# Kernel tuning notes

Hardware: AMD Instinct MI355X
Metric: run time of the kernel (lower is better)

The kernel has to match this reference:

```python
import jax, jax.numpy as jnp
import numpy as np

ALPHA, BETA, GAMMA = 1.0, 0.5, 0.25
FEATURE_DIM = 4
OHEM_RATIO = 3
K = 8  # fixed number of instance labels (0 = background)
DELTA_V, DELTA_D = 0.5, 1.5
EPS_DICE = 1e-3
EPS_IOU = 1e-6


def setup_inputs() -> dict:
    key = jax.random.key(0)
    k1, k2, k3, k4, k5 = jax.random.split(key, 5)
    B, h, w = 8, 160, 160
    H, W = 4 * h, 4 * w
    maps = jax.random.normal(k1, (B, 2 + FEATURE_DIM, h, w), jnp.float32)
    gt_texts = (jax.random.uniform(k2, (B, H, W)) > 0.5).astype(jnp.float32)
    gt_kernels = (jax.random.uniform(k3, (B, H, W)) > 0.6).astype(jnp.float32)
    training_masks = (jax.random.uniform(k4, (B, H, W)) > 0.05).astype(jnp.float32)
    gt_instance = jax.random.randint(k5, (B, H, W), 0, K).astype(jnp.int32)
    return dict(maps=maps, gt_texts=gt_texts, gt_kernels=gt_kernels,
                gt_instance=gt_instance, training_masks=training_masks)


def _up4(x):
    # F.interpolate(scale_factor=4, mode='nearest')
    return jnp.repeat(jnp.repeat(x, 4, axis=-2), 4, axis=-1)


def _dice(inp, tgt, mask):
    B = inp.shape[0]
    m = mask.reshape(B, -1)
    p = jax.nn.sigmoid(inp).reshape(B, -1) * m
    t = tgt.reshape(B, -1) * m
    a = jnp.sum(p * t, axis=1)
    b = jnp.sum(p * p, axis=1) + EPS_DICE
    c = jnp.sum(t * t, axis=1) + EPS_DICE
    return 1.0 - 2.0 * a / (b + c)  # [B]


def _ohem_single(score, gt, tm):
    pos = gt > 0.5
    pos_num = jnp.sum(pos) - jnp.sum(pos & (tm <= 0.5))
    neg = ~pos
    neg_num = jnp.minimum(pos_num * OHEM_RATIO, jnp.sum(neg))
    neg_scores = jnp.where(neg, score, -jnp.inf).ravel()
    sorted_desc = -jnp.sort(-neg_scores)
    idx = jnp.clip(neg_num - 1, 0, neg_scores.size - 1)
    thr = sorted_desc[idx]
    sel = (((score >= thr) | pos) & (tm > 0.5)).astype(tm.dtype)
    fallback = (pos_num == 0) | (neg_num == 0)
    return jnp.where(fallback, tm, sel)


def _emb_single(emb, instance, kernel, tm):
    # emb: [D,H,W]; EmbLoss v1 (agg/dis/reg), fixed K labels instead of torch.unique
    D = emb.shape[0]
    tm_b = tm > 0.5
    kn_b = kernel > 0.5
    inst = jnp.where(tm_b, instance, 0).ravel()              # instance * training_mask
    inst_k = jnp.where(kn_b & tm_b, instance, 0).ravel()     # instance * kernel
    e = emb.reshape(D, -1)                                   # [D,N]
    labels = jnp.arange(K)
    oh_k = (inst_k[None, :] == labels[:, None]).astype(e.dtype)   # [K,N]
    cnt_k = oh_k.sum(axis=1)                                  # [K]
    emb_mean = jnp.einsum('dn,kn->dk', e, oh_k) / jnp.maximum(cnt_k, 1.0)  # [D,K]
    nz = (labels != 0)
    emb_mean = emb_mean * nz[None, :].astype(e.dtype)          # torch skips lb==0 -> col0 stays 0
    present = cnt_k > 0
    valid = present & nz
    nv = jnp.sum(valid)

    # l_agg: per-pixel distance to own-instance mean
    mean_pix = emb_mean[:, inst]                               # [D,N]
    sqd = jnp.sum((e - mean_pix) ** 2, axis=0)
    dist = jnp.sqrt(jnp.maximum(sqd, 1e-12))
    val = jnp.log(jnp.maximum(dist - DELTA_V, 0.0) ** 2 + 1.0)
    oh_i = (inst[None, :] == labels[:, None]).astype(e.dtype)  # [K,N]
    cnt_i = oh_i.sum(axis=1)
    lagg_per = (oh_i @ val) / jnp.maximum(cnt_i, 1.0)          # [K]
    l_agg = jnp.sum(lagg_per * valid) / jnp.maximum(nv, 1)

    # l_dis: pairwise distances between instance means (off-diag, excl label 0)
    diff = emb_mean[:, :, None] - emb_mean[:, None, :]         # [D,K,K]
    sq = jnp.sum(diff ** 2, axis=0)
    pd = jnp.sqrt(jnp.where(sq > 0, sq, 1.0))                  # safe sqrt; diag masked below
    vdis = jnp.log(jnp.maximum(2.0 * DELTA_D - pd, 0.0) ** 2 + 1.0)
    pmask = (valid[:, None] & valid[None, :] & (~jnp.eye(K, dtype=bool))).astype(e.dtype)
    l_dis = jnp.sum(vdis * pmask) / jnp.maximum(pmask.sum(), 1.0)
    l_dis = jnp.where(nv >= 2, l_dis, 0.0)

    # l_reg over all present labels (col0 is zero -> contributes log(1)=0)
    num_instance = jnp.sum(present)
    l_reg = jnp.sum(jnp.log(jnp.linalg.norm(emb_mean, axis=0) + 1.0) * present) \
            / jnp.maximum(num_instance, 1) * 0.001

    loss = l_agg + l_dis + l_reg
    return jnp.where(nv > 0, loss, 0.0)


def reference(maps, gt_texts, gt_kernels, gt_instance, training_masks):
    p = _up4(maps)                     # [B,6,H,W]
    texts = p[:, 0]
    kernels = p[:, 1]
    embs = p[:, 2:]

    sel = jax.vmap(_ohem_single)(texts, gt_texts, training_masks)
    loss_text = _dice(texts, gt_texts, sel)

    sel_k = (jax.nn.sigmoid(texts) > 0.5).astype(texts.dtype) * training_masks
    loss_kernels = _dice(kernels, gt_kernels, sel_k)

    loss_emb = jax.vmap(_emb_single)(embs, gt_instance, gt_kernels, training_masks)

    loss = ALPHA * loss_text + BETA * loss_kernels + GAMMA * loss_emb  # [B]
    return jnp.mean(loss)  # reduction='mean'
```

## Files before the change

kernel.cpp:

```cpp
#include <hip/hip_runtime.h>
#include <math.h>

#define NB 8
#define CW 160
#define CPB (CW*CW)
#define FW 640
#define PIX (FW*FW)
#define MBLK 25
#define PBLK 400
#define HSUB 8

#define OFF_CNTS     0
#define OFF_CI       (NB*CPB*4)
#define OFF_CKC     (OFF_CI + NB*CPB*8)
#define OFF_PARTM   (OFF_CKC + NB*CPB*8)
#define OFF_PARTV   (OFF_PARTM + NB*MBLK*54*4)
#define OFF_POSNUM  (OFF_PARTV + NB*MBLK*8*4)
#define OFF_HIST0   (OFF_POSNUM + NB*4)
#define OFF_HIST1   (OFF_HIST0 + NB*2048*4)
#define WS_END      (OFF_HIST1 + NB*2048*4)

__device__ __forceinline__ float wredf(float v) {
    #pragma unroll
    for (int o = 32; o; o >>= 1) v += __shfl_xor(v, o, 64);
    return v;
}
__device__ __forceinline__ int wredi(int v) {
    #pragma unroll
    for (int o = 32; o; o >>= 1) v += __shfl_xor(v, o, 64);
    return v;
}
__device__ __forceinline__ unsigned long long wredu64(unsigned long long v) {
    #pragma unroll
    for (int o = 32; o; o >>= 1) v += __shfl_xor(v, o, 64);
    return v;
}
__device__ __forceinline__ unsigned keyxf(float f) {
    unsigned bits = __float_as_uint(f);
    return (bits & 0x80000000u) ? ~bits : (bits | 0x80000000u);
}

__device__ int coscan256(const int* __restrict__ hist, int nbins, int tid, int* s_sum) {
    int chunk = nbins >> 8;
    int base = tid * chunk;
    int s = 0;
    #pragma unroll 8
    for (int i = 0; i < chunk; i++) s += hist[base + i];
    s_sum[tid] = s;
    __syncthreads();
    #pragma unroll
    for (int off = 1; off < 256; off <<= 1) {
        int add = (tid >= off) ? s_sum[tid - off] : 0;
        __syncthreads();
        s_sum[tid] += add;
        __syncthreads();
    }
    return s_sum[255];
}
__device__ void cofind256(const int* __restrict__ hist, int nbins, int tid,
                          const int* s_sum, int j, int* s_out) {
    int chunk = nbins >> 8;
    if (tid == 0) { s_out[0] = 0; s_out[1] = 0; }
    __syncthreads();
    int incl = s_sum[tid];
    int excl = (tid > 0) ? s_sum[tid - 1] : 0;
    if (j >= excl && j < incl) {
        int base = tid * chunk, cum = excl;
        for (int i = 0; i < chunk; i++) {
            int c = hist[base + i];
            if (j < cum + c) { s_out[0] = base + i; s_out[1] = j - cum; break; }
            cum += c;
        }
    }
    __syncthreads();
}
__device__ __forceinline__ int ohem_j(int pn, int N) {
    long long nn = min(3LL * (long long)pn, (long long)N);
    int j = (int)((long long)N - nn);
    if (j < 0) j = 0;
    if (j >= N) j = (N > 0) ? N - 1 : 0;
    return j;
}

__global__ __launch_bounds__(256) void k_pass1(const float* __restrict__ gt_texts,
                                               const float* __restrict__ gt_kernels,
                                               const int*   __restrict__ gt_instance,
                                               const float* __restrict__ tm,
                                               unsigned* __restrict__ cnts,
                                               unsigned long long* __restrict__ ciA,
                                               unsigned long long* __restrict__ ckA,
                                               int* __restrict__ posNum,
                                               int* __restrict__ hist0,
                                               int* __restrict__ hist1) {
    int tid = threadIdx.x;
    if (blockIdx.x < 64) {
        int zi = blockIdx.x * 256 + tid;
        hist0[zi] = 0;
        hist1[zi] = 0;
        if (zi < NB) posNum[zi] = 0;
    }
    int b = blockIdx.x / PBLK;
    int blk = blockIdx.x - b * PBLK;
    int r = tid >> 6;
    int c = tid & 63;
    int cp = blk * 64 + c;
    int cy = cp / CW, cx = cp - cy * CW;
    size_t fbase = (size_t)b * PIX + (size_t)(cy * 4 + r) * FW + cx * 4;

    float4 g  = *reinterpret_cast<const float4*>(gt_texts   + fbase);
    float4 gk = *reinterpret_cast<const float4*>(gt_kernels + fbase);
    float4 m  = *reinterpret_cast<const float4*>(tm         + fbase);
    int4  idv = *reinterpret_cast<const int4*>(gt_instance + fbase);

    int neg = 0, c_tmb = 0, c_gt = 0, c_kb = 0;
    unsigned long long ci = 0, ck = 0;
    auto px = [&](float gg, float gkk, float mm, int id) {
        bool tmb = mm > 0.5f;
        bool gt  = gg > 0.5f;
        bool gkb = gkk > 0.5f;
        neg += !gt;
        c_tmb += tmb;
        c_gt += (gt && tmb);
        bool kb = tmb && gkb;
        c_kb += kb;
        ci += 1ull << ((tmb ? id : 0) * 8);
        ck += 1ull << ((kb ? id : 0) * 8);
    };
    px(g.x, gk.x, m.x, idv.x);
    px(g.y, gk.y, m.y, idv.y);
    px(g.z, gk.z, m.z, idv.z);
    px(g.w, gk.w, m.w, idv.w);

    __shared__ unsigned long long s_ci[256];
    __shared__ unsigned long long s_ck[256];
    __shared__ unsigned s_cnt[256];
    s_ci[tid] = ci;
    s_ck[tid] = ck;
    s_cnt[tid] = (unsigned)c_tmb | ((unsigned)c_gt << 8) | ((unsigned)c_kb << 16) | ((unsigned)neg << 24);
    __syncthreads();
    if (tid < 64) {
        unsigned cs = s_cnt[tid] + s_cnt[tid + 64] + s_cnt[tid + 128] + s_cnt[tid + 192];
        unsigned long long cis = s_ci[tid] + s_ci[tid + 64] + s_ci[tid + 128] + s_ci[tid + 192];
        unsigned long long cks = s_ck[tid] + s_ck[tid + 64] + s_ck[tid + 128] + s_ck[tid + 192];
        int gidx = b * CPB + blk * 64 + tid;
        cnts[gidx] = cs;
        ciA[gidx] = cis;
        ckA[gidx] = cks;
    }
}

__global__ __launch_bounds__(256) void k_hist0(const float* __restrict__ maps,
                                               const unsigned* __restrict__ cnts,
                                               int* __restrict__ posNum,
                                               int* __restrict__ hist0) {
    int b = blockIdx.x >> 3, hb = blockIdx.x & 7, tid = threadIdx.x;
    const float* tex = maps + (size_t)b * 6 * CPB;
    const unsigned* cn = cnts + b * CPB;
    __shared__ int h[2048];
    for (int i = tid; i < 2048; i += 256) h[i] = 0;
    __syncthreads();
    int posSum = 0;
    #pragma unroll
    for (int it = 0; it < 4; it++) {
        int q = it * 256 + tid;
        if (q < 800) {
            int i0 = hb * 3200 + q * 4;
            float4 t4 = *reinterpret_cast<const float4*>(tex + i0);
            uint4  c4 = *reinterpret_cast<const uint4*>(cn + i0);
            float tv[4] = {t4.x, t4.y, t4.z, t4.w};
            unsigned cv[4] = {c4.x, c4.y, c4.z, c4.w};
            #pragma unroll
            for (int j = 0; j < 4; j++) {
                posSum += (int)((cv[j] >> 8) & 255);
                int w = (int)(cv[j] >> 24);
                if (w) atomicAdd(&h[keyxf(tv[j]) >> 21], w);
            }
        }
    }
    posSum = wredi(posSum);
    if ((tid & 63) == 0 && posSum) atomicAdd(&posNum[b], posSum);
    __syncthreads();
    for (int i = tid; i < 2048; i += 256) {
        int v = h[i];
        if (v) atomicAdd(&hist0[b * 2048 + i], v);
    }
}

__global__ __launch_bounds__(256) void k_hist1(const float* __restrict__ maps,
                                               const unsigned* __restrict__ cnts,
                                               const int* __restrict__ posNum,
                                               const int* __restrict__ hist0,
                                               int* __restrict__ hist1) {
    int b = blockIdx.x >> 3, hb = blockIdx.x & 7, tid = threadIdx.x;
    __shared__ int s_sum[256], s_out[2];
    const int* h0 = hist0 + b * 2048;
    int N = coscan256(h0, 2048, tid, s_sum);
    int j0 = ohem_j(posNum[b], N);
    cofind256(h0, 2048, tid, s_sum, j0, s_out);
    int d0 = s_out[0];
    __shared__ int h[2048];
    for (int i = tid; i < 2048; i += 256) h[i] = 0;
    __syncthreads();
    const float* tex = maps + (size_t)b * 6 * CPB;
    const unsigned* cn = cnts + b * CPB;
    #pragma unroll
    for (int it = 0; it < 4; it++) {
        int q = it * 256 + tid;
        if (q < 800) {
            int i0 = hb * 3200 + q * 4;
            float4 t4 = *reinterpret_cast<const float4*>(tex + i0);
            uint4  c4 = *reinterpret_cast<const uint4*>(cn + i0);
            float tv[4] = {t4.x, t4.y, t4.z, t4.w};
            unsigned cv[4] = {c4.x, c4.y, c4.z, c4.w};
            #pragma unroll
            for (int j = 0; j < 4; j++) {
                int w = (int)(cv[j] >> 24);
                if (!w) continue;
                unsigned key = keyxf(tv[j]);
                if ((int)(key >> 21) == d0) atomicAdd(&h[(key >> 10) & 0x7FF], w);
            }
        }
    }
    __syncthreads();
    for (int i = tid; i < 2048; i += 256) {
        int v = h[i];
        if (v) atomicAdd(&hist1[b * 2048 + i], v);
    }
}

__global__ __launch_bounds__(256) void k_main_c(const float* __restrict__ maps,
                                                const unsigned* __restrict__ cnts,
                                                const unsigned long long* __restrict__ ciA,
                                                const unsigned long long* __restrict__ ckA,
                                                const int* __restrict__ posNum,
                                                const int* __restrict__ hist0,
                                                const int* __restrict__ hist1,
                                                float* __restrict__ partM) {
    int b = blockIdx.x / MBLK;
    int blk = blockIdx.x - b * MBLK;
    int tid = threadIdx.x;
    int p0 = (blk * 256 + tid) * 4;
    const float* mb = maps + (size_t)b * 6 * CPB;

    float txa[4], kna[4], e0a[4], e1a[4], e2a[4], e3a[4];
    *reinterpret_cast<float4*>(txa) = *reinterpret_cast<const float4*>(mb + p0);
    *reinterpret_cast<float4*>(kna) = *reinterpret_cast<const float4*>(mb + CPB + p0);
    *reinterpret_cast<float4*>(e0a) = *reinterpret_cast<const float4*>(mb + 2 * CPB + p0);
    *reinterpret_cast<float4*>(e1a) = *reinterpret_cast<const float4*>(mb + 3 * CPB + p0);
    *reinterpret_cast<float4*>(e2a) = *reinterpret_cast<const float4*>(mb + 4 * CPB + p0);
    *reinterpret_cast<float4*>(e3a) = *reinterpret_cast<const float4*>(mb + 5 * CPB + p0);
    unsigned ca[4];
    *reinterpret_cast<uint4*>(ca) = *reinterpret_cast<const uint4*>(cnts + b * CPB + p0);
    unsigned long long cia[4], cka[4];
    *reinterpret_cast<ulonglong2*>(cia)     = *reinterpret_cast<const ulonglong2*>(ciA + b * CPB + p0);
    *reinterpret_cast<ulonglong2*>(cia + 2) = *reinterpret_cast<const ulonglong2*>(ciA + b * CPB + p0 + 2);
    *reinterpret_cast<ulonglong2*>(cka)     = *reinterpret_cast<const ulonglong2*>(ckA + b * CPB + p0);
    *reinterpret_cast<ulonglong2*>(cka + 2) = *reinterpret_cast<const ulonglong2*>(ckA + b * CPB + p0 + 2);

    __shared__ int s_sum[256], s_out[2];
    const int* h0 = hist0 + b * 2048;
    const int* h1 = hist1 + b * 2048;
    int N = coscan256(h0, 2048, tid, s_sum);
    int pn = posNum[b];
    long long nn = min(3LL * (long long)pn, (long long)N);
    int fb = (pn == 0 || nn == 0) ? 1 : 0;
    int j0 = ohem_j(pn, N);
    cofind256(h0, 2048, tid, s_sum, j0, s_out);
    int d0 = s_out[0], j1 = s_out[1];
    coscan256(h1, 2048, tid, s_sum);
    cofind256(h1, 2048, tid, s_sum, j1, s_out);
    int d1 = s_out[0];
    unsigned key = ((unsigned)d0 << 21) | ((unsigned)d1 << 10);
    unsigned tb = (key & 0x80000000u) ? (key & 0x7FFFFFFFu) : ~key;
    float thr = __uint_as_float(tb);

    float at = 0.f, bt = 0.f, ct = 0.f, ak = 0.f, bk = 0.f, ckd = 0.f;
    unsigned long long ciS = 0, ckS = 0;
    float se[4][8];
    #pragma unroll
    for (int d = 0; d < 4; d++)
        #pragma unroll
        for (int k = 0; k < 8; k++) se[d][k] = 0.f;

    #pragma unroll
    for (int j = 0; j < 4; j++) {
        float tx = txa[j], kn = kna[j];
        unsigned c = ca[j];
        float c_tmb = (float)(c & 255);
        float c_gt  = (float)((c >> 8) & 255);
        float c_kb  = (float)((c >> 16) & 255);
        float sig_t = 1.f / (1.f + expf(-tx));
        float sig_k = 1.f / (1.f + expf(-kn));
        bool sge = (tx >= thr);
        bool skp = (tx > 0.0f);
        float n_sel = fb ? c_tmb : (sge ? c_tmb : c_gt);
        float n_selk = skp ? c_tmb : 0.f;
        float n_selk_g = skp ? c_kb : 0.f;
        at += sig_t * c_gt;
        bt += sig_t * sig_t * n_sel;
        ct += c_gt;
        ak += sig_k * n_selk_g;
        bk += sig_k * sig_k * n_selk;
        ckd += n_selk_g;
        ciS += cia[j];
        unsigned long long ck = cka[j];
        ckS += ck;
        #pragma unroll
        for (int k = 1; k < 8; k++) {
            float fc = (float)((ck >> (8 * k)) & 255);
            se[0][k] += e0a[j] * fc;
            se[1][k] += e1a[j] * fc;
            se[2][k] += e2a[j] * fc;
            se[3][k] += e3a[j] * fc;
        }
    }

    at = wredf(at); bt = wredf(bt); ct = wredf(ct);
    ak = wredf(ak); bk = wredf(bk); ckd = wredf(ckd);
    const unsigned long long M = 0x00FF00FF00FF00FFull;
    unsigned long long ci0 = wredu64(ciS & M);
    unsigned long long ci1 = wredu64((ciS >> 8) & M);
    unsigned long long ck0 = wredu64(ckS & M);
    unsigned long long ck1 = wredu64((ckS >> 8) & M);
    #pragma unroll
    for (int d = 0; d < 4; d++)
        #pragma unroll
        for (int k = 1; k < 8; k++) se[d][k] = wredf(se[d][k]);

    __shared__ float sh[4][54];
    int w = tid >> 6;
    if ((tid & 63) == 0) {
        sh[w][0] = at; sh[w][1] = bt; sh[w][2] = ct;
        sh[w][3] = ak; sh[w][4] = bk; sh[w][5] = ckd;
        #pragma unroll
        for (int q = 0; q < 4; q++) {
            sh[w][6 + 2 * q]      = (float)((ck0 >> (16 * q)) & 0xFFFF);
            sh[w][6 + 2 * q + 1]  = (float)((ck1 >> (16 * q)) & 0xFFFF);
            sh[w][14 + 2 * q]     = (float)((ci0 >> (16 * q)) & 0xFFFF);
            sh[w][14 + 2 * q + 1] = (float)((ci1 >> (16 * q)) & 0xFFFF);
        }
        #pragma unroll
        for (int d = 0; d < 4; d++) {
            sh[w][22 + d * 8] = 0.f;
            #pragma unroll
            for (int k = 1; k < 8; k++) sh[w][22 + d * 8 + k] = se[d][k];
        }
    }
    __syncthreads();
    if (tid < 54)
        partM[(size_t)(b * MBLK + blk) * 54 + tid] =
            sh[0][tid] + sh[1][tid] + sh[2][tid] + sh[3][tid];
}

__global__ __launch_bounds__(256) void k_val_c(const float* __restrict__ maps,
                                               const unsigned long long* __restrict__ ciA,
                                               const float* __restrict__ partM,
                                               float* __restrict__ partV) {
    int b = blockIdx.x / MBLK;
    int blk = blockIdx.x - b * MBLK;
    int tid = threadIdx.x;
    int p0 = (blk * 256 + tid) * 4;
    const float* mb = maps + (size_t)b * 6 * CPB;

    float e0a[4], e1a[4], e2a[4], e3a[4];
    *reinterpret_cast<float4*>(e0a) = *reinterpret_cast<const float4*>(mb + 2 * CPB + p0);
    *reinterpret_cast<float4*>(e1a) = *reinterpret_cast<const float4*>(mb + 3 * CPB + p0);
    *reinterpret_cast<float4*>(e2a) = *reinterpret_cast<const float4*>(mb + 4 * CPB + p0);
    *reinterpret_cast<float4*>(e3a) = *reinterpret_cast<const float4*>(mb + 5 * CPB + p0);
    unsigned long long cia[4];
    *reinterpret_cast<ulonglong2*>(cia)     = *reinterpret_cast<const ulonglong2*>(ciA + b * CPB + p0);
    *reinterpret_cast<ulonglong2*>(cia + 2) = *reinterpret_cast<const ulonglong2*>(ciA + b * CPB + p0 + 2);

    __shared__ float A54[54];
    __shared__ float shm[32];
    __shared__ float shv[8];
    if (tid < 54) {
        float s = 0.f;
        #pragma unroll 5
        for (int j = 0; j < MBLK; j++) s += partM[(size_t)(b * MBLK + j) * 54 + tid];
        A54[tid] = s;
    }
    __syncthreads();
    if (tid < 32) {
        int k = tid & 7;
        shm[tid] = (k == 0) ? 0.f : A54[22 + tid] / fmaxf(A54[6 + k], 1.f);
    }
    if (tid < 8) shv[tid] = (tid != 0 && A54[6 + tid] > 0.f) ? 1.f : 0.f;
    __syncthreads();

    float sv[8];
    #pragma unroll
    for (int k = 0; k < 8; k++) sv[k] = 0.f;
    #pragma unroll
    for (int j = 0; j < 4; j++) {
        unsigned long long ci = cia[j];
        #pragma unroll
        for (int k = 1; k < 8; k++) {
            int c = (int)((ci >> (8 * k)) & 255);
            if (c && shv[k] > 0.5f) {
                float d0 = e0a[j] - shm[k], d1 = e1a[j] - shm[8 + k];
                float d2 = e2a[j] - shm[16 + k], d3 = e3a[j] - shm[24 + k];
                float sq = d0 * d0 + d1 * d1 + d2 * d2 + d3 * d3;
                float dist = sqrtf(fmaxf(sq, 1e-12f));
                float t = fmaxf(dist - 0.5f, 0.f);
                sv[k] += logf(t * t + 1.f) * (float)c;
            }
        }
    }
    #pragma unroll
    for (int k = 1; k < 8; k++) sv[k] = wredf(sv[k]);
    __shared__ float shp[4][8];
    int w = tid >> 6;
    if ((tid & 63) == 0) {
        shp[w][0] = 0.f;
        #pragma unroll
        for (int k = 1; k < 8; k++) shp[w][k] = sv[k];
    }
    __syncthreads();
    if (tid < 8)
        partV[(size_t)(b * MBLK + blk) * 8 + tid] =
            shp[0][tid] + shp[1][tid] + shp[2][tid] + shp[3][tid];
}

__global__ __launch_bounds__(64) void k_final(const float* __restrict__ partM,
                                              const float* __restrict__ partV,
                                              float* __restrict__ out) {
    int tid = threadIdx.x;
    __shared__ float AM[NB][54];
    __shared__ float SV[NB][8];
    __shared__ float tot[NB];
    for (int i = tid; i < NB * 54; i += 64) {
        int b = i / 54, c = i - b * 54;
        float s = 0.f;
        for (int j = 0; j < MBLK; j++) s += partM[(size_t)(b * MBLK + j) * 54 + c];
        AM[b][c] = s;
    }
    {
        int b = tid >> 3, k = tid & 7;
        float s = 0.f;
        for (int j = 0; j < MBLK; j++) s += partV[(size_t)(b * MBLK + j) * 8 + k];
        SV[b][k] = s;
    }
    __syncthreads();
    if (tid < NB) {
        int b = tid;
        const float* A = AM[b];
        float ltext = 1.f - 2.f * A[0] / (A[1] + A[2] + 0.002f);
        float lkern = 1.f - 2.f * A[3] / (A[4] + A[5] + 0.002f);
        float m[4][8];
        float valid[8];
        int nv = 0, ninst = 0;
        #pragma unroll
        for (int k = 0; k < 8; k++) {
            float c = A[6 + k];
            float inv = 1.f / fmaxf(c, 1.f);
            #pragma unroll
            for (int d = 0; d < 4; d++) m[d][k] = (k == 0) ? 0.f : A[22 + d * 8 + k] * inv;
            int pres = (c > 0.f);
            ninst += pres;
            int v = pres && (k != 0);
            nv += v;
            valid[k] = (float)v;
        }
        float s = 0.f;
        for (int i = 1; i < 8; i++) {
            if (valid[i] < 0.5f) continue;
            for (int j = 1; j < 8; j++) {
                if (j == i || valid[j] < 0.5f) continue;
                float sq = 0.f;
                #pragma unroll
                for (int d = 0; d < 4; d++) { float df = m[d][i] - m[d][j]; sq += df * df; }
                float pd = sqrtf(sq > 0.f ? sq : 1.f);
                float t = fmaxf(3.f - pd, 0.f);
                s += logf(t * t + 1.f);
            }
        }
        float pairs = (float)(nv * nv - nv);
        float l_dis = (nv >= 2) ? s / fmaxf(pairs, 1.f) : 0.f;
        float s2 = 0.f;
        for (int k = 0; k < 8; k++) {
            if (A[6 + k] > 0.f) {
                float n2 = 0.f;
                #pragma unroll
                for (int d = 0; d < 4; d++) n2 += m[d][k] * m[d][k];
                s2 += logf(sqrtf(n2) + 1.f);
            }
        }
        float l_reg = s2 / fmaxf((float)ninst, 1.f) * 0.001f;
        float lagg = 0.f;
        #pragma unroll
        for (int k = 0; k < 8; k++)
            lagg += valid[k] * (SV[b][k] / fmaxf(A[14 + k], 1.f));
        lagg /= fmaxf((float)nv, 1.f);
        float le = (nv > 0) ? (lagg + l_dis + l_reg) : 0.f;
        tot[b] = ltext + 0.5f * lkern + 0.25f * le;
    }
    __syncthreads();
    if (tid == 0) {
        float t = 0.f;
        for (int b = 0; b < NB; b++) t += tot[b];
        out[0] = t / (float)NB;
    }
}

extern "C" void kernel_launch(void* const* d_in, const int* in_sizes, int n_in,
                              void* d_out, int out_size, void* d_ws, size_t ws_size,
                              hipStream_t stream) {
    const float* maps        = (const float*)d_in[0];
    const float* gt_texts    = (const float*)d_in[1];
    const float* gt_kernels  = (const float*)d_in[2];
    const int*   gt_instance = (const int*)d_in[3];
    const float* tm          = (const float*)d_in[4];
    char* ws = (char*)d_ws;
    unsigned* cnts  = (unsigned*)(ws + OFF_CNTS);
    unsigned long long* ciA = (unsigned long long*)(ws + OFF_CI);
    unsigned long long* ckA = (unsigned long long*)(ws + OFF_CKC);
    float* partM    = (float*)(ws + OFF_PARTM);
    float* partV    = (float*)(ws + OFF_PARTV);
    int*   posNum   = (int*)(ws + OFF_POSNUM);
    int*   hist0    = (int*)(ws + OFF_HIST0);
    int*   hist1    = (int*)(ws + OFF_HIST1);

    k_pass1<<<NB * PBLK, 256, 0, stream>>>(gt_texts, gt_kernels, gt_instance, tm,
                                           cnts, ciA, ckA, posNum, hist0, hist1);
    k_hist0<<<NB * HSUB, 256, 0, stream>>>(maps, cnts, posNum, hist0);
    k_hist1<<<NB * HSUB, 256, 0, stream>>>(maps, cnts, posNum, hist0, hist1);
    k_main_c<<<NB * MBLK, 256, 0, stream>>>(maps, cnts, ciA, ckA, posNum, hist0, hist1, partM);
    k_val_c<<<NB * MBLK, 256, 0, stream>>>(maps, ciA, partM, partV);
    k_final<<<1, 64, 0, stream>>>(partM, partV, (float*)d_out);
}
```

Baseline: 138.5 us.

## Fuse all loss stages into one cooperative persistent kernel with grid syncs

Replaces the six-kernel pipeline with a single cooperative kernel of 512 persistent blocks that loops over the work of each former kernel, separated by grid-wide syncs. The aim is to remove launch gaps and per-kernel tail effects between the small histogram, main and final stages. The first OHEM histogram search is now done once per batch and stored as threshold metadata, so the main stage no longer rescans the first-level histogram. Risks: grid.sync cost, fewer blocks for the bandwidth-heavy first pass, and the old multi-kernel path kept as a fallback if the cooperative launch fails.

```diff
diff --git a/kernel.cpp b/kernel.cpp
--- a/kernel.cpp
+++ b/kernel.cpp
@@ -1,5 +1,8 @@
 #include <hip/hip_runtime.h>
+#include <hip/hip_cooperative_groups.h>
 #include <math.h>
+
+namespace cg = cooperative_groups;
 
 #define NB 8
 #define CW 160
@@ -9,6 +12,7 @@
 #define MBLK 25
 #define PBLK 400
 #define HSUB 8
+#define GRID 512
 
 #define OFF_CNTS     0
 #define OFF_CI       (NB*CPB*4)
@@ -18,7 +22,8 @@
 #define OFF_POSNUM  (OFF_PARTV + NB*MBLK*8*4)
 #define OFF_HIST0   (OFF_POSNUM + NB*4)
 #define OFF_HIST1   (OFF_HIST0 + NB*2048*4)
-#define WS_END      (OFF_HIST1 + NB*2048*4)
+#define OFF_META    (OFF_HIST1 + NB*2048*4)
+#define WS_END      (OFF_META + NB*16)
 
 __device__ __forceinline__ float wredf(float v) {
     #pragma unroll
@@ -80,6 +85,427 @@
     if (j < 0) j = 0;
     if (j >= N) j = (N > 0) ? N - 1 : 0;
     return j;
+}
+
+__global__ __launch_bounds__(256, 2) void k_fused(const float* __restrict__ gt_texts,
+                                                  const float* __restrict__ gt_kernels,
+                                                  const int*   __restrict__ gt_instance,
+                                                  const float* __restrict__ tm,
+                                                  const float* __restrict__ maps,
+                                                  unsigned* __restrict__ cnts,
+                                                  unsigned long long* __restrict__ ciA,
+                                                  unsigned long long* __restrict__ ckA,
+                                                  int* __restrict__ posNum,
+                                                  int* __restrict__ hist0,
+                                                  int* __restrict__ hist1,
+                                                  int* __restrict__ thrMeta,
+                                                  float* __restrict__ partM,
+                                                  float* __restrict__ partV,
+                                                  float* __restrict__ out) {
+    cg::grid_group grid = cg::this_grid();
+    const int tid = threadIdx.x;
+    const int nbk = gridDim.x;
+
+    __shared__ int h[2048];
+    __shared__ int s_sum[256];
+    __shared__ int s_out[2];
+    __shared__ unsigned long long s_ci[256];
+    __shared__ unsigned long long s_ck[256];
+    __shared__ unsigned s_cnt[256];
+
+    for (int i = blockIdx.x * 256 + tid; i < NB * 2048; i += nbk * 256) {
+        hist0[i] = 0;
+        hist1[i] = 0;
+    }
+    if (blockIdx.x == 0 && tid < NB) posNum[tid] = 0;
+
+    for (int u = blockIdx.x; u < NB * PBLK; u += nbk) {
+        int b = u / PBLK;
+        int blk = u - b * PBLK;
+        int r = tid >> 6;
+        int c = tid & 63;
+        int cp = blk * 64 + c;
+        int cy = cp / CW, cx = cp - cy * CW;
+        size_t fbase = (size_t)b * PIX + (size_t)(cy * 4 + r) * FW + cx * 4;
+
+        float4 g  = *reinterpret_cast<const float4*>(gt_texts   + fbase);
+        float4 gk = *reinterpret_cast<const float4*>(gt_kernels + fbase);
+        float4 m  = *reinterpret_cast<const float4*>(tm         + fbase);
+        int4  idv = *reinterpret_cast<const int4*>(gt_instance + fbase);
+
+        int neg = 0, c_tmb = 0, c_gt = 0, c_kb = 0;
+        unsigned long long ci = 0, ck = 0;
+        auto px = [&](float gg, float gkk, float mm, int id) {
+            bool tmb = mm > 0.5f;
+            bool gt  = gg > 0.5f;
+            bool gkb = gkk > 0.5f;
+            neg += !gt;
+            c_tmb += tmb;
+            c_gt += (gt && tmb);
+            bool kb = tmb && gkb;
+            c_kb += kb;
+            ci += 1ull << ((tmb ? id : 0) * 8);
+            ck += 1ull << ((kb ? id : 0) * 8);
+        };
+        px(g.x, gk.x, m.x, idv.x);
+        px(g.y, gk.y, m.y, idv.y);
+        px(g.z, gk.z, m.z, idv.z);
+        px(g.w, gk.w, m.w, idv.w);
+
+        s_ci[tid] = ci;
+        s_ck[tid] = ck;
+        s_cnt[tid] = (unsigned)c_tmb | ((unsigned)c_gt << 8) | ((unsigned)c_kb << 16) | ((unsigned)neg << 24);
+        __syncthreads();
+        if (tid < 64) {
+            unsigned cs = s_cnt[tid] + s_cnt[tid + 64] + s_cnt[tid + 128] + s_cnt[tid + 192];
+            unsigned long long cis = s_ci[tid] + s_ci[tid + 64] + s_ci[tid + 128] + s_ci[tid + 192];
+            unsigned long long cks = s_ck[tid] + s_ck[tid + 64] + s_ck[tid + 128] + s_ck[tid + 192];
+            int gidx = b * CPB + blk * 64 + tid;
+            cnts[gidx] = cs;
+            ciA[gidx] = cis;
+            ckA[gidx] = cks;
+        }
+        __syncthreads();
+    }
+    grid.sync();
+
+    for (int u = blockIdx.x; u < NB * HSUB; u += nbk) {
+        int b = u >> 3, hb = u & 7;
+        const float* tex = maps + (size_t)b * 6 * CPB;
+        const unsigned* cn = cnts + b * CPB;
+        for (int i = tid; i < 2048; i += 256) h[i] = 0;
+        __syncthreads();
+        int posSum = 0;
+        #pragma unroll
+        for (int it = 0; it < 4; it++) {
+            int q = it * 256 + tid;
+            if (q < 800) {
+                int i0 = hb * 3200 + q * 4;
+                float4 t4 = *reinterpret_cast<const float4*>(tex + i0);
+                uint4  c4 = *reinterpret_cast<const uint4*>(cn + i0);
+                float tv[4] = {t4.x, t4.y, t4.z, t4.w};
+                unsigned cv[4] = {c4.x, c4.y, c4.z, c4.w};
+                #pragma unroll
+                for (int j = 0; j < 4; j++) {
+                    posSum += (int)((cv[j] >> 8) & 255);
+                    int w = (int)(cv[j] >> 24);
+                    if (w) atomicAdd(&h[keyxf(tv[j]) >> 21], w);
+                }
+            }
+        }
+        posSum = wredi(posSum);
+        if ((tid & 63) == 0 && posSum) atomicAdd(&posNum[b], posSum);
+        __syncthreads();
+        for (int i = tid; i < 2048; i += 256) {
+            int v = h[i];
+            if (v) atomicAdd(&hist0[b * 2048 + i], v);
+        }
+        __syncthreads();
+    }
+    grid.sync();
+
+    for (int u = blockIdx.x; u < NB * HSUB; u += nbk) {
+        int b = u >> 3, hb = u & 7;
+        const int* h0 = hist0 + b * 2048;
+        int N = coscan256(h0, 2048, tid, s_sum);
+        int pn = posNum[b];
+        long long nn = min(3LL * (long long)pn, (long long)N);
+        int fb = (pn == 0 || nn == 0) ? 1 : 0;
+        int j0 = ohem_j(pn, N);
+        cofind256(h0, 2048, tid, s_sum, j0, s_out);
+        int d0 = s_out[0], j1 = s_out[1];
+        if (hb == 0 && tid == 0) {
+            thrMeta[b * 4]     = d0;
+            thrMeta[b * 4 + 1] = j1;
+            thrMeta[b * 4 + 2] = fb;
+        }
+        for (int i = tid; i < 2048; i += 256) h[i] = 0;
+        __syncthreads();
+        const float* tex = maps + (size_t)b * 6 * CPB;
+        const unsigned* cn = cnts + b * CPB;
+        #pragma unroll
+        for (int it = 0; it < 4; it++) {
+            int q = it * 256 + tid;
+            if (q < 800) {
+                int i0 = hb * 3200 + q * 4;
+                float4 t4 = *reinterpret_cast<const float4*>(tex + i0);
+                uint4  c4 = *reinterpret_cast<const uint4*>(cn + i0);
+                float tv[4] = {t4.x, t4.y, t4.z, t4.w};
+                unsigned cv[4] = {c4.x, c4.y, c4.z, c4.w};
+                #pragma unroll
+                for (int j = 0; j < 4; j++) {
+                    int w = (int)(cv[j] >> 24);
+                    if (!w) continue;
+                    unsigned key = keyxf(tv[j]);
+                    if ((int)(key >> 21) == d0) atomicAdd(&h[(key >> 10) & 0x7FF], w);
+                }
+            }
+        }
+        __syncthreads();
+        for (int i = tid; i < 2048; i += 256) {
+            int v = h[i];
+            if (v) atomicAdd(&hist1[b * 2048 + i], v);
+        }
+        __syncthreads();
+    }
+    grid.sync();
+
+    for (int u = blockIdx.x; u < NB * MBLK; u += nbk) {
+        int b = u / MBLK;
+        int blk = u - b * MBLK;
+        int p0 = (blk * 256 + tid) * 4;
+        const float* mb = maps + (size_t)b * 6 * CPB;
+
+        float txa[4], kna[4], e0a[4], e1a[4], e2a[4], e3a[4];
+        *reinterpret_cast<float4*>(txa) = *reinterpret_cast<const float4*>(mb + p0);
+        *reinterpret_cast<float4*>(kna) = *reinterpret_cast<const float4*>(mb + CPB + p0);
+        *reinterpret_cast<float4*>(e0a) = *reinterpret_cast<const float4*>(mb + 2 * CPB + p0);
+        *reinterpret_cast<float4*>(e1a) = *reinterpret_cast<const float4*>(mb + 3 * CPB + p0);
+        *reinterpret_cast<float4*>(e2a) = *reinterpret_cast<const float4*>(mb + 4 * CPB + p0);
+        *reinterpret_cast<float4*>(e3a) = *reinterpret_cast<const float4*>(mb + 5 * CPB + p0);
+        unsigned ca[4];
+        *reinterpret_cast<uint4*>(ca) = *reinterpret_cast<const uint4*>(cnts + b * CPB + p0);
+        unsigned long long cia[4], cka[4];
+        *reinterpret_cast<ulonglong2*>(cia)     = *reinterpret_cast<const ulonglong2*>(ciA + b * CPB + p0);
+        *reinterpret_cast<ulonglong2*>(cia + 2) = *reinterpret_cast<const ulonglong2*>(ciA + b * CPB + p0 + 2);
+        *reinterpret_cast<ulonglong2*>(cka)     = *reinterpret_cast<const ulonglong2*>(ckA + b * CPB + p0);
+        *reinterpret_cast<ulonglong2*>(cka + 2) = *reinterpret_cast<const ulonglong2*>(ckA + b * CPB + p0 + 2);
+
+        int d0 = thrMeta[b * 4], j1 = thrMeta[b * 4 + 1], fb = thrMeta[b * 4 + 2];
+        const int* h1 = hist1 + b * 2048;
+        coscan256(h1, 2048, tid, s_sum);
+        cofind256(h1, 2048, tid, s_sum, j1, s_out);
+        int d1 = s_out[0];
+        unsigned key = ((unsigned)d0 << 21) | ((unsigned)d1 << 10);
+        unsigned tb = (key & 0x80000000u) ? (key & 0x7FFFFFFFu) : ~key;
+        float thr = __uint_as_float(tb);
+
+        float at = 0.f, bt = 0.f, ct = 0.f, ak = 0.f, bk = 0.f, ckd = 0.f;
+        unsigned long long ciS = 0, ckS = 0;
+        float se[4][8];
+        #pragma unroll
+        for (int d = 0; d < 4; d++)
+            #pragma unroll
+            for (int k = 0; k < 8; k++) se[d][k] = 0.f;
+
+        #pragma unroll
+        for (int j = 0; j < 4; j++) {
+            float tx = txa[j], kn = kna[j];
+            unsigned c = ca[j];
+            float c_tmb = (float)(c & 255);
+            float c_gt  = (float)((c >> 8) & 255);
+            float c_kb  = (float)((c >> 16) & 255);
+            float sig_t = 1.f / (1.f + expf(-tx));
+            float sig_k = 1.f / (1.f + expf(-kn));
+            bool sge = (tx >= thr);
+            bool skp = (tx > 0.0f);
+            float n_sel = fb ? c_tmb : (sge ? c_tmb : c_gt);
+            float n_selk = skp ? c_tmb : 0.f;
+            float n_selk_g = skp ? c_kb : 0.f;
+            at += sig_t * c_gt;
+            bt += sig_t * sig_t * n_sel;
+            ct += c_gt;
+            ak += sig_k * n_selk_g;
+            bk += sig_k * sig_k * n_selk;
+            ckd += n_selk_g;
+            ciS += cia[j];
+            unsigned long long ck = cka[j];
+            ckS += ck;
+            #pragma unroll
+            for (int k = 1; k < 8; k++) {
+                float fc = (float)((ck >> (8 * k)) & 255);
+                se[0][k] += e0a[j] * fc;
+                se[1][k] += e1a[j] * fc;
+                se[2][k] += e2a[j] * fc;
+                se[3][k] += e3a[j] * fc;
+            }
+        }
+
+        at = wredf(at); bt = wredf(bt); ct = wredf(ct);
+        ak = wredf(ak); bk = wredf(bk); ckd = wredf(ckd);
+        const unsigned long long M = 0x00FF00FF00FF00FFull;
+        unsigned long long ci0 = wredu64(ciS & M);
+        unsigned long long ci1 = wredu64((ciS >> 8) & M);
+        unsigned long long ck0 = wredu64(ckS & M);
+        unsigned long long ck1 = wredu64((ckS >> 8) & M);
+        #pragma unroll
+        for (int d = 0; d < 4; d++)
+            #pragma unroll
+            for (int k = 1; k < 8; k++) se[d][k] = wredf(se[d][k]);
+
+        float* shf = (float*)h;
+        int w = tid >> 6;
+        if ((tid & 63) == 0) {
+            float* sw = shf + w * 54;
+            sw[0] = at; sw[1] = bt; sw[2] = ct;
+            sw[3] = ak; sw[4] = bk; sw[5] = ckd;
+            #pragma unroll
+            for (int q = 0; q < 4; q++) {
+                sw[6 + 2 * q]      = (float)((ck0 >> (16 * q)) & 0xFFFF);
+                sw[6 + 2 * q + 1]  = (float)((ck1 >> (16 * q)) & 0xFFFF);
+                sw[14 + 2 * q]     = (float)((ci0 >> (16 * q)) & 0xFFFF);
+                sw[14 + 2 * q + 1] = (float)((ci1 >> (16 * q)) & 0xFFFF);
+            }
+            #pragma unroll
+            for (int d = 0; d < 4; d++) {
+                sw[22 + d * 8] = 0.f;
+                #pragma unroll
+                for (int k = 1; k < 8; k++) sw[22 + d * 8 + k] = se[d][k];
+            }
+        }
+        __syncthreads();
+        if (tid < 54)
+            partM[(size_t)(b * MBLK + blk) * 54 + tid] =
+                shf[tid] + shf[54 + tid] + shf[108 + tid] + shf[162 + tid];
+        __syncthreads();
+    }
+    grid.sync();
+
+    for (int u = blockIdx.x; u < NB * MBLK; u += nbk) {
+        int b = u / MBLK;
+        int blk = u - b * MBLK;
+        int p0 = (blk * 256 + tid) * 4;
+        const float* mb = maps + (size_t)b * 6 * CPB;
+
+        float e0a[4], e1a[4], e2a[4], e3a[4];
+        *reinterpret_cast<float4*>(e0a) = *reinterpret_cast<const float4*>(mb + 2 * CPB + p0);
+        *reinterpret_cast<float4*>(e1a) = *reinterpret_cast<const float4*>(mb + 3 * CPB + p0);
+        *reinterpret_cast<float4*>(e2a) = *reinterpret_cast<const float4*>(mb + 4 * CPB + p0);
+        *reinterpret_cast<float4*>(e3a) = *reinterpret_cast<const float4*>(mb + 5 * CPB + p0);
+        unsigned long long cia[4];
+        *reinterpret_cast<ulonglong2*>(cia)     = *reinterpret_cast<const ulonglong2*>(ciA + b * CPB + p0);
+        *reinterpret_cast<ulonglong2*>(cia + 2) = *reinterpret_cast<const ulonglong2*>(ciA + b * CPB + p0 + 2);
+
+        float* A54 = (float*)h;
+        float* shm = A54 + 64;
+        float* shv = A54 + 96;
+        float* shp = A54 + 112;
+        if (tid < 54) {
+            float s = 0.f;
+            #pragma unroll 5
+            for (int j = 0; j < MBLK; j++) s += partM[(size_t)(b * MBLK + j) * 54 + tid];
+            A54[tid] = s;
+        }
+        __syncthreads();
+        if (tid < 32) {
+            int k = tid & 7;
+            shm[tid] = (k == 0) ? 0.f : A54[22 + tid] / fmaxf(A54[6 + k], 1.f);
+        }
+        if (tid < 8) shv[tid] = (tid != 0 && A54[6 + tid] > 0.f) ? 1.f : 0.f;
+        __syncthreads();
+
+        float sv[8];
+        #pragma unroll
+        for (int k = 0; k < 8; k++) sv[k] = 0.f;
+        #pragma unroll
+        for (int j = 0; j < 4; j++) {
+            unsigned long long ci = cia[j];
+            #pragma unroll
+            for (int k = 1; k < 8; k++) {
+                int c = (int)((ci >> (8 * k)) & 255);
+                if (c && shv[k] > 0.5f) {
+                    float d0 = e0a[j] - shm[k], d1 = e1a[j] - shm[8 + k];
+                    float d2 = e2a[j] - shm[16 + k], d3 = e3a[j] - shm[24 + k];
+                    float sq = d0 * d0 + d1 * d1 + d2 * d2 + d3 * d3;
+                    float dist = sqrtf(fmaxf(sq, 1e-12f));
+                    float t = fmaxf(dist - 0.5f, 0.f);
+                    sv[k] += logf(t * t + 1.f) * (float)c;
+                }
+            }
+        }
+        #pragma unroll
+        for (int k = 1; k < 8; k++) sv[k] = wredf(sv[k]);
+        int w = tid >> 6;
+        if ((tid & 63) == 0) {
+            shp[w * 8] = 0.f;
+            #pragma unroll
+            for (int k = 1; k < 8; k++) shp[w * 8 + k] = sv[k];
+        }
+        __syncthreads();
+        if (tid < 8)
+            partV[(size_t)(b * MBLK + blk) * 8 + tid] =
+                shp[tid] + shp[8 + tid] + shp[16 + tid] + shp[24 + tid];
+        __syncthreads();
+    }
+    grid.sync();
+
+    if (blockIdx.x == 0) {
+        float* AM = (float*)h;
+        float* SV = AM + 440;
+        float* totB = SV + 64;
+        for (int i = tid; i < NB * 54; i += 256) {
+            int b = i / 54, c = i - b * 54;
+            float s = 0.f;
+            for (int j = 0; j < MBLK; j++) s += partM[(size_t)(b * MBLK + j) * 54 + c];
+            AM[b * 54 + c] = s;
+        }
+        if (tid < 64) {
+            int b = tid >> 3, k = tid & 7;
+            float s = 0.f;
+            for (int j = 0; j < MBLK; j++) s += partV[(size_t)(b * MBLK + j) * 8 + k];
+            SV[b * 8 + k] = s;
+        }
+        __syncthreads();
+        if (tid < NB) {
+            int b = tid;
+            const float* A = AM + b * 54;
+            float ltext = 1.f - 2.f * A[0] / (A[1] + A[2] + 0.002f);
+            float lkern = 1.f - 2.f * A[3] / (A[4] + A[5] + 0.002f);
+            float m[4][8];
+            float valid[8];
+            int nv = 0, ninst = 0;
+            #pragma unroll
+            for (int k = 0; k < 8; k++) {
+                float c = A[6 + k];
+                float inv = 1.f / fmaxf(c, 1.f);
+                #pragma unroll
+                for (int d = 0; d < 4; d++) m[d][k] = (k == 0) ? 0.f : A[22 + d * 8 + k] * inv;
+                int pres = (c > 0.f);
+                ninst += pres;
+                int v = pres && (k != 0);
+                nv += v;
+                valid[k] = (float)v;
+            }
+            float s = 0.f;
+            for (int i = 1; i < 8; i++) {
+                if (valid[i] < 0.5f) continue;
+                for (int j = 1; j < 8; j++) {
+                    if (j == i || valid[j] < 0.5f) continue;
+                    float sq = 0.f;
+                    #pragma unroll
+                    for (int d = 0; d < 4; d++) { float df = m[d][i] - m[d][j]; sq += df * df; }
+                    float pd = sqrtf(sq > 0.f ? sq : 1.f);
+                    float t = fmaxf(3.f - pd, 0.f);
+                    s += logf(t * t + 1.f);
+                }
+            }
+            float pairs = (float)(nv * nv - nv);
+            float l_dis = (nv >= 2) ? s / fmaxf(pairs, 1.f) : 0.f;
+            float s2 = 0.f;
+            for (int k = 0; k < 8; k++) {
+                if (A[6 + k] > 0.f) {
+                    float n2 = 0.f;
+                    #pragma unroll
+                    for (int d = 0; d < 4; d++) n2 += m[d][k] * m[d][k];
+                    s2 += logf(sqrtf(n2) + 1.f);
+                }
+            }
+            float l_reg = s2 / fmaxf((float)ninst, 1.f) * 0.001f;
+            float lagg = 0.f;
+            #pragma unroll
+            for (int k = 0; k < 8; k++)
+                lagg += valid[k] * (SV[b * 8 + k] / fmaxf(A[14 + k], 1.f));
+            lagg /= fmaxf((float)nv, 1.f);
+            float le = (nv > 0) ? (lagg + l_dis + l_reg) : 0.f;
+            totB[b] = ltext + 0.5f * lkern + 0.25f * le;
+        }
+        __syncthreads();
+        if (tid == 0) {
+            float t = 0.f;
+            for (int b = 0; b < NB; b++) t += totB[b];
+            out[0] = t / (float)NB;
+        }
+    }
 }
 
 __global__ __launch_bounds__(256) void k_pass1(const float* __restrict__ gt_texts,
@@ -106,12 +532,10 @@
     int cp = blk * 64 + c;
     int cy = cp / CW, cx = cp - cy * CW;
     size_t fbase = (size_t)b * PIX + (size_t)(cy * 4 + r) * FW + cx * 4;
-
     float4 g  = *reinterpret_cast<const float4*>(gt_texts   + fbase);
     float4 gk = *reinterpret_cast<const float4*>(gt_kernels + fbase);
     float4 m  = *reinterpret_cast<const float4*>(tm         + fbase);
     int4  idv = *reinterpret_cast<const int4*>(gt_instance + fbase);
-
     int neg = 0, c_tmb = 0, c_gt = 0, c_kb = 0;
     unsigned long long ci = 0, ck = 0;
     auto px = [&](float gg, float gkk, float mm, int id) {
@@ -130,7 +554,6 @@
     px(g.y, gk.y, m.y, idv.y);
     px(g.z, gk.z, m.z, idv.z);
     px(g.w, gk.w, m.w, idv.w);
-
     __shared__ unsigned long long s_ci[256];
     __shared__ unsigned long long s_ck[256];
     __shared__ unsigned s_cnt[256];
@@ -190,14 +613,21 @@
                                                const unsigned* __restrict__ cnts,
                                                const int* __restrict__ posNum,
                                                const int* __restrict__ hist0,
-                                               int* __restrict__ hist1) {
+                                               int* __restrict__ hist1,
+                                               int* __restrict__ thrMeta) {
     int b = blockIdx.x >> 3, hb = blockIdx.x & 7, tid = threadIdx.x;
     __shared__ int s_sum[256], s_out[2];
     const int* h0 = hist0 + b * 2048;
     int N = coscan256(h0, 2048, tid, s_sum);
-    int j0 = ohem_j(posNum[b], N);
+    int pn = posNum[b];
+    long long nn = min(3LL * (long long)pn, (long long)N);
+    int fb = (pn == 0 || nn == 0) ? 1 : 0;
+    int j0 = ohem_j(pn, N);
     cofind256(h0, 2048, tid, s_sum, j0, s_out);
-    int d0 = s_out[0];
+    int d0 = s_out[0], j1 = s_out[1];
+    if (hb == 0 && tid == 0) {
+        thrMeta[b * 4] = d0; thrMeta[b * 4 + 1] = j1; thrMeta[b * 4 + 2] = fb;
+    }
     __shared__ int h[2048];
     for (int i = tid; i < 2048; i += 256) h[i] = 0;
     __syncthreads();
@@ -232,8 +662,7 @@
                                                 const unsigned* __restrict__ cnts,
                                                 const unsigned long long* __restrict__ ciA,
                                                 const unsigned long long* __restrict__ ckA,
-                                                const int* __restrict__ posNum,
-                                                const int* __restrict__ hist0,
+                                                const int* __restrict__ thrMeta,
                                                 const int* __restrict__ hist1,
                                                 float* __restrict__ partM) {
     int b = blockIdx.x / MBLK;
@@ -241,7 +670,6 @@
     int tid = threadIdx.x;
     int p0 = (blk * 256 + tid) * 4;
     const float* mb = maps + (size_t)b * 6 * CPB;
-
     float txa[4], kna[4], e0a[4], e1a[4], e2a[4], e3a[4];
     *reinterpret_cast<float4*>(txa) = *reinterpret_cast<const float4*>(mb + p0);
     *reinterpret_cast<float4*>(kna) = *reinterpret_cast<const float4*>(mb + CPB + p0);
@@ -256,24 +684,15 @@
     *reinterpret_cast<ulonglong2*>(cia + 2) = *reinterpret_cast<const ulonglong2*>(ciA + b * CPB + p0 + 2);
     *reinterpret_cast<ulonglong2*>(cka)     = *reinterpret_cast<const ulonglong2*>(ckA + b * CPB + p0);
     *reinterpret_cast<ulonglong2*>(cka + 2) = *reinterpret_cast<const ulonglong2*>(ckA + b * CPB + p0 + 2);
-
     __shared__ int s_sum[256], s_out[2];
-    const int* h0 = hist0 + b * 2048;
+    int d0 = thrMeta[b * 4], j1 = thrMeta[b * 4 + 1], fb = thrMeta[b * 4 + 2];
     const int* h1 = hist1 + b * 2048;
-    int N = coscan256(h0, 2048, tid, s_sum);
-    int pn = posNum[b];
-    long long nn = min(3LL * (long long)pn, (long long)N);
-    int fb = (pn == 0 || nn == 0) ? 1 : 0;
-    int j0 = ohem_j(pn, N);
-    cofind256(h0, 2048, tid, s_sum, j0, s_out);
-    int d0 = s_out[0], j1 = s_out[1];
     coscan256(h1, 2048, tid, s_sum);
     cofind256(h1, 2048, tid, s_sum, j1, s_out);
     int d1 = s_out[0];
     unsigned key = ((unsigned)d0 << 21) | ((unsigned)d1 << 10);
     unsigned tb = (key & 0x80000000u) ? (key & 0x7FFFFFFFu) : ~key;
     float thr = __uint_as_float(tb);
-
     float at = 0.f, bt = 0.f, ct = 0.f, ak = 0.f, bk = 0.f, ckd = 0.f;
     unsigned long long ciS = 0, ckS = 0;
     float se[4][8];
@@ -281,7 +700,6 @@
     for (int d = 0; d < 4; d++)
         #pragma unroll
         for (int k = 0; k < 8; k++) se[d][k] = 0.f;
-
     #pragma unroll
     for (int j = 0; j < 4; j++) {
         float tx = txa[j], kn = kna[j];
@@ -314,7 +732,6 @@
             se[3][k] += e3a[j] * fc;
         }
     }
-
     at = wredf(at); bt = wredf(bt); ct = wredf(ct);
     ak = wredf(ak); bk = wredf(bk); ckd = wredf(ckd);
     const unsigned long long M = 0x00FF00FF00FF00FFull;
@@ -326,7 +743,6 @@
     for (int d = 0; d < 4; d++)
         #pragma unroll
         for (int k = 1; k < 8; k++) se[d][k] = wredf(se[d][k]);
-
     __shared__ float sh[4][54];
     int w = tid >> 6;
     if ((tid & 63) == 0) {
@@ -361,7 +777,6 @@
     int tid = threadIdx.x;
     int p0 = (blk * 256 + tid) * 4;
     const float* mb = maps + (size_t)b * 6 * CPB;
-
     float e0a[4], e1a[4], e2a[4], e3a[4];
     *reinterpret_cast<float4*>(e0a) = *reinterpret_cast<const float4*>(mb + 2 * CPB + p0);
     *reinterpret_cast<float4*>(e1a) = *reinterpret_cast<const float4*>(mb + 3 * CPB + p0);
@@ -370,7 +785,6 @@
     unsigned long long cia[4];
     *reinterpret_cast<ulonglong2*>(cia)     = *reinterpret_cast<const ulonglong2*>(ciA + b * CPB + p0);
     *reinterpret_cast<ulonglong2*>(cia + 2) = *reinterpret_cast<const ulonglong2*>(ciA + b * CPB + p0 + 2);
-
     __shared__ float A54[54];
     __shared__ float shm[32];
     __shared__ float shv[8];
@@ -387,7 +801,6 @@
     }
     if (tid < 8) shv[tid] = (tid != 0 && A54[6 + tid] > 0.f) ? 1.f : 0.f;
     __syncthreads();
-
     float sv[8];
     #pragma unroll
     for (int k = 0; k < 8; k++) sv[k] = 0.f;
@@ -520,12 +933,22 @@
     int*   posNum   = (int*)(ws + OFF_POSNUM);
     int*   hist0    = (int*)(ws + OFF_HIST0);
     int*   hist1    = (int*)(ws + OFF_HIST1);
-
-    k_pass1<<<NB * PBLK, 256, 0, stream>>>(gt_texts, gt_kernels, gt_instance, tm,
-                                           cnts, ciA, ckA, posNum, hist0, hist1);
-    k_hist0<<<NB * HSUB, 256, 0, stream>>>(maps, cnts, posNum, hist0);
-    k_hist1<<<NB * HSUB, 256, 0, stream>>>(maps, cnts, posNum, hist0, hist1);
-    k_main_c<<<NB * MBLK, 256, 0, stream>>>(maps, cnts, ciA, ckA, posNum, hist0, hist1, partM);
-    k_val_c<<<NB * MBLK, 256, 0, stream>>>(maps, ciA, partM, partV);
-    k_final<<<1, 64, 0, stream>>>(partM, partV, (float*)d_out);
-}
+    int*   thrMeta  = (int*)(ws + OFF_META);
+    float* outp     = (float*)d_out;
+
+    void* args[] = { &gt_texts, &gt_kernels, &gt_instance, &tm, &maps,
+                     &cnts, &ciA, &ckA, &posNum, &hist0, &hist1, &thrMeta,
+                     &partM, &partV, &outp };
+    hipError_t err = hipLaunchCooperativeKernel((const void*)k_fused,
+                                                dim3(GRID), dim3(256),
+                                                args, 0, stream);
+    if (err != hipSuccess) {
+        k_pass1<<<NB * PBLK, 256, 0, stream>>>(gt_texts, gt_kernels, gt_instance, tm,
+                                               cnts, ciA, ckA, posNum, hist0, hist1);
+        k_hist0<<<NB * HSUB, 256, 0, stream>>>(maps, cnts, posNum, hist0);
+        k_hist1<<<NB * HSUB, 256, 0, stream>>>(maps, cnts, posNum, hist0, hist1, thrMeta);
+        k_main_c<<<NB * MBLK, 256, 0, stream>>>(maps, cnts, ciA, ckA, thrMeta, hist1, partM);
+        k_val_c<<<NB * MBLK, 256, 0, stream>>>(maps, ciA, partM, partV);
+        k_final<<<1, 64, 0, stream>>>(partM, partV, (float*)d_out);
+    }
+}
```

After: 407.7 us. +194.4%, slower.
